# Kernel tuning notes

Hardware: AMD Instinct MI355X
Metric: run time of the kernel (lower is better)

The kernel has to match this reference:

```python
import jax, jax.numpy as jnp
import numpy as np

NH, HD, MB = 32, 64, 16        # heads, head_dim, TTT mini-batch size
BASE_LR = 1.0
ROPE_THETA = 10000.0


def _ln(x, w, b, eps):
    mu = x.mean(-1, keepdims=True)
    var = ((x - mu) ** 2).mean(-1, keepdims=True)
    return (x - mu) / jnp.sqrt(var + eps) * w + b


def _rotate_half(x):
    x1, x2 = jnp.split(x, 2, axis=-1)
    return jnp.concatenate([-x2, x1], axis=-1)


def _ln_l2_bwd(x, target, g, b, eps=1e-6):
    # grad of ||LN(x)*g+b - target||^2 / 2 wrt x (fused, as in ttt-lm)
    D = x.shape[-1]
    mu = x.mean(-1, keepdims=True)
    var = ((x - mu) ** 2).mean(-1, keepdims=True)
    std = jnp.sqrt(var + eps)
    xh = (x - mu) / std
    gxh = (g * xh + b - target) * g
    return (D * gxh - gxh.sum(-1, keepdims=True) - xh * (gxh * xh).sum(-1, keepdims=True)) / (D * std)


def _ttt_forward(x, q_w, k_w, v_w, o_w, ttt_lr_w, ttt_lr_b, token_idx_off,
                 ttt_norm_w, ttt_norm_b, W1, b1, post_w, post_b):
    B, L, C = x.shape
    NM = L // MB
    XQ = (x @ q_w).reshape(B, L, NH, HD).transpose(0, 2, 1, 3)  # [B,NH,L,HD]
    XK = (x @ k_w).reshape(B, L, NH, HD).transpose(0, 2, 1, 3)
    XV = (x @ v_w).reshape(B, L, NH, HD).transpose(0, 2, 1, 3)
    # rotary embedding at position_ids % mini_batch_size
    pos = (jnp.arange(L) % MB).astype(jnp.float32)
    inv = 1.0 / (ROPE_THETA ** (jnp.arange(0, HD, 2, dtype=jnp.float32) / HD))
    fr = pos[:, None] * inv[None, :]
    emb = jnp.concatenate([fr, fr], axis=-1)           # [L,HD]
    cos, sin = jnp.cos(emb), jnp.sin(emb)
    XQ = XQ * cos + _rotate_half(XQ) * sin
    XK = XK * cos + _rotate_half(XK) * sin
    # learning-rate gate (eta)
    Xm = x.reshape(B, NM, MB, C)
    ttt_lr = jax.nn.sigmoid(jnp.einsum('bnkc,hdc->bhnkd', Xm, ttt_lr_w)
                            + ttt_lr_b.reshape(1, NH, 1, 1, 1))       # [B,NH,NM,MB,1]
    ttt_lr_eta = BASE_LR * ttt_lr.transpose(0, 1, 2, 4, 3) / HD       # [B,NH,NM,1,MB]
    tok = jnp.maximum(1.0 / jnp.arange(1, MB + 1, dtype=jnp.float32) + token_idx_off, 0.0)
    eta = tok.reshape(1, 1, 1, MB, 1) * ttt_lr_eta                    # [B,NH,NM,MB,MB]

    def tomb(t):  # [B,NH,L,HD] -> [NM,B,NH,MB,HD]
        return t.reshape(B, NH, NM, MB, HD).transpose(2, 0, 1, 3, 4)

    xs = (tomb(XQ), tomb(XK), tomb(XV), eta.transpose(2, 0, 1, 3, 4))
    lw = ttt_norm_w.reshape(1, NH, 1, HD)
    lb = ttt_norm_b.reshape(1, NH, 1, HD)
    tril = jnp.tril(jnp.ones((MB, MB), x.dtype))
    W1s = jnp.broadcast_to(W1, (B, NH, HD, HD)).astype(x.dtype)
    b1s = jnp.broadcast_to(b1, (B, NH, 1, HD)).astype(x.dtype)

    def step(carry, xs_t):
        W1c, b1c = carry
        xq, xk, xv, et = xs_t                      # [B,NH,MB,HD], et [B,NH,MB,MB]
        Z1 = xk @ W1c + b1c
        grad = _ln_l2_bwd(Z1, xv - xk, lw, lb)     # grad of per-head TTT loss wrt Z1
        Attn1 = jnp.tril(xq @ xk.transpose(0, 1, 3, 2))
        b1_bar = b1c - (et * tril) @ grad
        Z1_bar = xq @ W1c - (et * Attn1) @ grad + b1_bar
        last_eta = et[:, :, -1, :, None]           # [B,NH,MB,1]
        W1n = W1c - jnp.einsum('bhki,bhkj->bhij', last_eta * xk, grad)
        b1n = b1c - (last_eta * grad).sum(-2, keepdims=True)
        out = xq + _ln(Z1_bar, lw, lb, 1e-6)
        return (W1n, b1n), out

    _, outs = jax.lax.scan(step, (W1s, b1s), xs)   # outs: [NM,B,NH,MB,HD]
    y = outs.transpose(1, 0, 3, 2, 4).reshape(B, L, C)
    y = _ln(y, post_w, post_b, 1e-6)
    return y @ o_w


def setup_inputs() -> dict:
    key = jax.random.key(0)
    ks = jax.random.split(key, 16)
    B, L, C, DH = 4, 2048, 2048, 1024
    s = 0.02
    return {
        'enc_input': jax.random.normal(ks[0], (B, L, C), jnp.float32),
        'ln1_w': jnp.ones((C,), jnp.float32), 'ln1_b': jnp.zeros((C,), jnp.float32),
        'q_w': jax.random.normal(ks[1], (C, C), jnp.float32) * s,
        'k_w': jax.random.normal(ks[2], (C, C), jnp.float32) * s,
        'v_w': jax.random.normal(ks[3], (C, C), jnp.float32) * s,
        'o_w': jax.random.normal(ks[4], (C, C), jnp.float32) * s,
        'ttt_lr_w': jax.random.normal(ks[5], (NH, 1, C), jnp.float32) * s,
        'ttt_lr_b': jax.random.normal(ks[6], (NH,), jnp.float32) * s,
        'token_idx_off': jax.random.normal(ks[7], (MB,), jnp.float32) * 0.01,
        'ttt_norm_w': jnp.ones((NH, HD), jnp.float32),
        'ttt_norm_b': jnp.zeros((NH, HD), jnp.float32),
        'W1': jax.random.normal(ks[8], (NH, HD, HD), jnp.float32) * s,
        'b1': jnp.zeros((NH, 1, HD), jnp.float32),
        'post_w': jnp.ones((C,), jnp.float32), 'post_b': jnp.zeros((C,), jnp.float32),
        'ffn_ln_w': jnp.ones((C,), jnp.float32), 'ffn_ln_b': jnp.zeros((C,), jnp.float32),
        'w1f': jax.random.normal(ks[9], (C, DH), jnp.float32) * s,
        'b1f': jnp.zeros((DH,), jnp.float32),
        'w2f': jax.random.normal(ks[10], (DH, C), jnp.float32) * s,
        'b2f': jnp.zeros((C,), jnp.float32),
    }


def reference(enc_input, ln1_w, ln1_b, q_w, k_w, v_w, o_w, ttt_lr_w, ttt_lr_b,
              token_idx_off, ttt_norm_w, ttt_norm_b, W1, b1, post_w, post_b,
              ffn_ln_w, ffn_ln_b, w1f, b1f, w2f, b2f):
    # pre-LN (torch default eps=1e-5) + TTT linear block + residual
    x = _ln(enc_input, ln1_w, ln1_b, 1e-5)
    y = _ttt_forward(x, q_w, k_w, v_w, o_w, ttt_lr_w, ttt_lr_b, token_idx_off,
                     ttt_norm_w, ttt_norm_b, W1, b1, post_w, post_b)
    y = y + enc_input
    # position-wise FFN (pre-LN eps=1e-6) + residual; dropout = eval no-op
    z = _ln(y, ffn_ln_w, ffn_ln_b, 1e-6)
    z = jax.nn.relu(z @ w1f + b1f) @ w2f + b2f
    return z + y
```

## Files before the change

### kernel.cpp

```cpp
#include <hip/hip_runtime.h>

typedef unsigned short u16;
typedef __attribute__((ext_vector_type(8))) short short8;
typedef __attribute__((ext_vector_type(8))) unsigned short ushort8;
typedef __attribute__((ext_vector_type(4))) unsigned short us4;
typedef __attribute__((ext_vector_type(4))) float f32x4;
typedef __attribute__((ext_vector_type(2))) float f32x2;
typedef __attribute__((ext_vector_type(2))) unsigned int uint2v;

#define DEV __device__ __forceinline__

DEV float bf2f(u16 u){ union{unsigned int i; float f;} v; v.i = ((unsigned int)u)<<16u; return v.f; }
DEV u16 f2bf(float f){ union{float f; unsigned int i;} v; v.f=f; unsigned int r = v.i + 0x7FFFu + ((v.i>>16)&1u); return (u16)(r>>16); }

DEV void gload16(const u16* g, u16* l){
  __builtin_amdgcn_global_load_lds((const __attribute__((address_space(1))) void*)g,
                                   (__attribute__((address_space(3))) void*)l, 16, 0, 0);
}

DEV float wsum(float v){
  v += __shfl_xor(v, 32, 64);
  v += __shfl_xor(v, 16, 64);
  v += __shfl_xor(v, 8, 64);
  v += __shfl_xor(v, 4, 64);
  v += __shfl_xor(v, 2, 64);
  v += __shfl_xor(v, 1, 64);
  return v;
}

#if __has_builtin(__builtin_amdgcn_permlane16_swap) && __has_builtin(__builtin_amdgcn_permlane32_swap)
DEV float qsum(float v){
  unsigned u = __float_as_uint(v);
  uint2v a = __builtin_amdgcn_permlane16_swap(u, u, false, false);
  float s = __uint_as_float(a[0]) + __uint_as_float(a[1]);
  unsigned u2 = __float_as_uint(s);
  uint2v bsw = __builtin_amdgcn_permlane32_swap(u2, u2, false, false);
  return __uint_as_float(bsw[0]) + __uint_as_float(bsw[1]);
}
#else
DEV float qsum(float v){
  v += __shfl_xor(v, 16, 64);
  v += __shfl_xor(v, 32, 64);
  return v;
}
#endif

DEV float swap32(float v){ return __shfl_xor(v, 32, 64); }

#define BARS() do{ asm volatile("s_waitcnt lgkmcnt(0)" ::: "memory"); \
  __builtin_amdgcn_s_barrier(); __builtin_amdgcn_sched_barrier(0); }while(0)

__global__ __launch_bounds__(256) void ln_row(
    const float* __restrict__ in, const float* __restrict__ w, const float* __restrict__ bb,
    float eps, u16* __restrict__ outb)
{
  const int wv = threadIdx.x>>6, lane = threadIdx.x&63;
  const int row = blockIdx.x*4 + wv;
  const float* p = in + (size_t)row*2048 + lane*4;
  f32x4 a[8];
  #pragma unroll
  for(int j=0;j<8;j++) a[j] = *(const f32x4*)(p + j*256);
  float s = 0.f;
  #pragma unroll
  for(int j=0;j<8;j++) s += a[j][0]+a[j][1]+a[j][2]+a[j][3];
  s = wsum(s);
  float mu = s*(1.f/2048.f);
  float vs = 0.f;
  #pragma unroll
  for(int j=0;j<8;j++)
    #pragma unroll
    for(int r=0;r<4;r++){ float d=a[j][r]-mu; vs += d*d; }
  vs = wsum(vs);
  float rstd = rsqrtf(vs*(1.f/2048.f) + eps);
  #pragma unroll
  for(int j=0;j<8;j++){
    f32x4 wj = *(const f32x4*)(w  + j*256 + lane*4);
    f32x4 bj = *(const f32x4*)(bb + j*256 + lane*4);
    us4 o;
    #pragma unroll
    for(int r=0;r<4;r++) o[r] = f2bf((a[j][r]-mu)*rstd*wj[r] + bj[r]);
    *(us4*)(outb + (size_t)row*2048 + j*256 + lane*4) = o;
  }
}

__global__ __launch_bounds__(256) void transpose_cast(
    const float* __restrict__ src, u16* __restrict__ dst, int K, int N)
{
  __shared__ float tile[32][33];
  const int kb = blockIdx.x*32, nb = blockIdx.y*32;
  const int tx = threadIdx.x & 31, ty = threadIdx.x >> 5;
  #pragma unroll
  for(int i=0;i<4;i++){
    int k = ty + i*8;
    tile[k][tx] = src[(size_t)(kb+k)*N + nb + tx];
  }
  __syncthreads();
  #pragma unroll
  for(int i=0;i<4;i++){
    int nn = ty + i*8;
    dst[(size_t)(nb+nn)*K + kb + tx] = f2bf(tile[tx][nn]);
  }
}

__global__ __launch_bounds__(256) void cast_lrw(const float* __restrict__ lrw, u16* __restrict__ dst)
{
  int i = blockIdx.x*256 + threadIdx.x;
  if (i < 32*2048) dst[i] = f2bf(lrw[i]);
  else dst[i] = 0;
}

__global__ void rope_init(const float* __restrict__ tio, float* __restrict__ cosb,
                          float* __restrict__ sinb, float* __restrict__ tokb)
{
  int t = blockIdx.x*256 + threadIdx.x;
  if (t < 1024){
    int p = t>>6, d = t&63;
    float inv = powf(10000.f, -(float)(2*(d&31))/64.f);
    float fr = (float)p * inv;
    cosb[t] = cosf(fr);
    sinb[t] = sinf(fr);
  }
  if (blockIdx.x==0 && threadIdx.x<16)
    tokb[threadIdx.x] = fmaxf(1.f/(float)(threadIdx.x+1) + tio[threadIdx.x], 0.f);
}

#define MM(MI,NI,AA,BB) acc[MI][NI] = __builtin_amdgcn_mfma_f32_16x16x32_bf16(AA, BB, acc[MI][NI], 0, 0, 0)

#define RD_A(D,KH,MF) (*(const short8*)(ldsb + ((D)<<16) + ((KH)<<14) + (wm<<13) + ((MF)<<10) + loff))
#define RD_B(D,KH,NF) (*(const short8*)(ldsb + ((D)<<16) + 32768 + ((KH)<<14) + (wn<<12) + ((NF)<<10) + loff))

#define PHASE(D,KH,MH,RB,STG,VM) { \
  __builtin_amdgcn_sched_barrier(0); \
  if (RB){ b0 = RD_B(D,KH,0); b1 = RD_B(D,KH,1); b2 = RD_B(D,KH,2); b3 = RD_B(D,KH,3); } \
  short8 a0 = RD_A(D,KH,4*(MH)+0); \
  short8 a1 = RD_A(D,KH,4*(MH)+1); \
  short8 a2 = RD_A(D,KH,4*(MH)+2); \
  short8 a3 = RD_A(D,KH,4*(MH)+3); \
  STG; \
  __builtin_amdgcn_sched_barrier(0); \
  __builtin_amdgcn_s_barrier(); \
  asm volatile("s_waitcnt lgkmcnt(0)" ::: "memory"); \
  __builtin_amdgcn_sched_barrier(0); \
  __builtin_amdgcn_s_setprio(1); \
  MM(4*(MH)+0,0,a0,b0); MM(4*(MH)+1,0,a1,b0); MM(4*(MH)+2,0,a2,b0); MM(4*(MH)+3,0,a3,b0); \
  MM(4*(MH)+0,1,a0,b1); MM(4*(MH)+1,1,a1,b1); MM(4*(MH)+2,1,a2,b1); MM(4*(MH)+3,1,a3,b1); \
  MM(4*(MH)+0,2,a0,b2); MM(4*(MH)+1,2,a1,b2); MM(4*(MH)+2,2,a2,b2); MM(4*(MH)+3,2,a3,b2); \
  MM(4*(MH)+0,3,a0,b3); MM(4*(MH)+1,3,a1,b3); MM(4*(MH)+2,3,a2,b3); MM(4*(MH)+3,3,a3,b3); \
  __builtin_amdgcn_s_setprio(0); \
  if (VM){ asm volatile("s_waitcnt vmcnt(8)" ::: "memory"); } \
  __builtin_amdgcn_sched_barrier(0); \
  __builtin_amdgcn_s_barrier(); \
}

template<int EPI>
__global__ __launch_bounds__(512, 2) void gemm256(
    const u16* __restrict__ A, const u16* __restrict__ Bt,
    float* __restrict__ C, u16* __restrict__ Cb,
    const float* __restrict__ bias, const float* __restrict__ resid,
    int Nld, int Nreal, int K, int ntN)
{
  extern __shared__ u16 lds[];
  const int t = threadIdx.x, lane = t&63, wv = t>>6;
  const int wm = wv>>2, wn = wv&3;
  const int fr = lane&15, kq = lane>>4;

  int bid = blockIdx.x;
  {
    int nwg = gridDim.x;
    int q = nwg>>3, r = nwg&7;
    int x = bid&7, l = bid>>3;
    bid = (x<r) ? (x*(q+1)+l) : (r*(q+1)+(x-r)*q+l);
  }
  const int bm = bid/ntN, bn = bid%ntN;

  f32x4 acc[8][4];
  #pragma unroll
  for(int i=0;i<8;i++)
    #pragma unroll
    for(int j=0;j<4;j++) acc[i][j]=(f32x4){0.f,0.f,0.f,0.f};

  const u16* gA = A  + (size_t)(bm*256)*K;
  const u16* gB = Bt + (size_t)(bn*256)*K;

  const int Ls   = (t&7) ^ ((t>>3)&7);
  const int rstg = ((t>>3)<<1) | (Ls>>2);
  const int cstg = (Ls&3)<<3;
  u16* const ldsw = lds + (wv<<9);

  const int Plane = (((fr&1)<<2) | kq) ^ (fr>>1);
  const int loff  = ((fr>>1)<<7) | (Plane<<4);
  const char* const ldsb = (const char*)lds;

  auto stA = [&](int d, int kh, int kts){
    u16* lb = ldsw + (d<<15) + (kh<<13);
    const u16* g = gA + (size_t)rstg*K + kts + (kh<<5) + cstg;
    gload16(g, lb);
    gload16(g + ((size_t)K<<7), lb + 4096);
  };
  auto stB = [&](int d, int kh, int kts){
    u16* lb = ldsw + (d<<15) + 16384 + (kh<<13);
    const u16* g = gB + (size_t)rstg*K + kts + (kh<<5) + cstg;
    gload16(g, lb);
    gload16(g + ((size_t)K<<7), lb + 4096);
  };

  stA(0,0,0); stB(0,0,0); stA(0,1,0); stB(0,1,0); stA(1,0,64); stB(1,0,64);
  asm volatile("s_waitcnt vmcnt(8)" ::: "memory");
  __builtin_amdgcn_sched_barrier(0);
  __builtin_amdgcn_s_barrier();

  for (int kt = 0; kt < K; kt += 128){
    const int ktp = (kt+128 < K) ? kt+128 : 0;
    const int ktq = (kt+192 < K) ? kt+192 : kt+192-K;
    short8 b0={0},b1={0},b2={0},b3={0};
    PHASE(0,0,0,1, stA(1,1,kt+64), 0)
    PHASE(0,0,1,0, stB(1,1,kt+64), 1)
    PHASE(0,1,0,1, stA(0,0,ktp),   0)
    PHASE(0,1,1,0, stB(0,0,ktp),   1)
    PHASE(1,0,0,1, stA(0,1,ktp),   0)
    PHASE(1,0,1,0, stB(0,1,ktp),   1)
    PHASE(1,1,0,1, stA(1,0,ktq),   0)
    PHASE(1,1,1,0, stB(1,0,ktq),   1)
  }

  const int cr = (lane>>4)<<2, cc = lane&15;
  #pragma unroll
  for(int mi=0;mi<8;mi++){
    #pragma unroll
    for(int ni=0;ni<4;ni++){
      const int row0 = bm*256 + wm*128 + mi*16 + cr;
      const int col  = bn*256 + wn*64  + ni*16 + cc;
      if (col < Nreal){
        #pragma unroll
        for(int rr=0;rr<4;rr++){
          size_t idx = (size_t)(row0+rr)*Nld + col;
          float v = acc[mi][ni][rr];
          if (EPI==1 || EPI==3) v += resid[idx];
          if (EPI==2 || EPI==3) v += bias[col];
          if (EPI==2){ v = fmaxf(v, 0.f); Cb[idx] = f2bf(v); }
          else if (EPI==4){ Cb[idx] = f2bf(v); }
          else C[idx] = v;
        }
      }
    }
  }
}

#define W1LD 72
#define XLD  72
#define GTLD 40
#define EKLD 40
#define EALD 40
#define TD2  68

__global__ __launch_bounds__(512, 1) void ttt_scan(
    const u16* __restrict__ XQKV,
    const float* __restrict__ ropec, const float* __restrict__ ropes,
    const float* __restrict__ tokp,
    const float* __restrict__ nw, const float* __restrict__ nb,
    const float* __restrict__ lrb,
    const float* __restrict__ W1i,
    const float* __restrict__ b1i,
    float* __restrict__ Y)
{
  const int blk = blockIdx.x, b = blk>>5, h = blk&31;
  const int t = threadIdx.x, lane = t&63, wv = t>>6;
  const int fr = lane&15, quad = lane>>4;
  const bool isStager = (wv==2)||(wv==3)||(wv==5)||(wv==6);
  const int sm = (wv>=5)? wv-3 : wv-2;

  __shared__ u16 W1bf[2][64*W1LD];
  __shared__ u16 xqbf[3][16*XLD];
  __shared__ u16 xkbf[3][16*XLD];
  __shared__ u16 exkT[3][64*EKLD];
  __shared__ u16 gradTbf[2][64*GTLD];
  __shared__ u16 etaA[2][16*EALD];
  __shared__ float tgT2[3][16*TD2];
  __shared__ float xqT2[3][16*TD2];
  __shared__ float b1s[64];
  __shared__ float lrs[3][16];

  const float lrbh = lrb[h];
  const float ct = tokp[15]*(1.f/64.f);
  const float sg = (lane<32)? -1.f : 1.f;

  f32x2 lwr[16];
  #pragma unroll
  for(int m=0;m<4;m++)
    #pragma unroll
    for(int r=0;r<4;r++){
      int d = m*16+quad*4+r;
      lwr[m*4+r] = (f32x2){nw[h*64+d], nb[h*64+d]};
    }
  float tki[4];
  #pragma unroll
  for(int r=0;r<4;r++) tki[r] = tokp[quad*4+r];

  float ccj[4], ssj[4];
  f32x4 wf0, wf1, wf2, wf3;
  u16 Pq[4], Pk[4], Pv[4], Pl[4];
  if (isStager){
    #pragma unroll
    for(int j=0;j<4;j++){
      ccj[j] = ropec[(sm*4+j)*64 + lane];
      ssj[j] = ropes[(sm*4+j)*64 + lane];
    }
    const float* wsrc = W1i + (size_t)h*4096;
    #pragma unroll
    for(int r=0;r<4;r++){
      int d = sm*16+quad*4+r;
      wf0[r] = wsrc[( 0+fr)*64 + d];
      wf1[r] = wsrc[(16+fr)*64 + d];
      wf2[r] = wsrc[(32+fr)*64 + d];
      wf3[r] = wsrc[(48+fr)*64 + d];
    }
    #pragma unroll
    for(int r=0;r<4;r++){
      int d = sm*16+quad*4+r;
      W1bf[0][d*W1LD +  0 + fr] = f2bf(wf0[r]);
      W1bf[0][d*W1LD + 16 + fr] = f2bf(wf1[r]);
      W1bf[0][d*W1LD + 32 + fr] = f2bf(wf2[r]);
      W1bf[0][d*W1LD + 48 + fr] = f2bf(wf3[r]);
    }
  }
  for(int i=t;i<64*24;i+=512){
    int rr=i/24, cp=16+i%24;
    gradTbf[0][rr*GTLD+cp]=0; gradTbf[1][rr*GTLD+cp]=0;
    exkT[0][rr*EKLD+cp]=0; exkT[1][rr*EKLD+cp]=0; exkT[2][rr*EKLD+cp]=0;
  }
  for(int i=t;i<16*24;i+=512){
    int rr=i/24, cp=16+i%24;
    etaA[0][rr*EALD+cp]=0; etaA[1][rr*EALD+cp]=0;
  }
  if (t<64) b1s[t]=b1i[h*64+t];

  auto loadP = [&](int n){
    const size_t rb = (size_t)b*2048 + n*16;
    #pragma unroll
    for(int j=0;j<4;j++){
      const u16* p = XQKV + (rb+sm*4+j)*6272 + h*64 + lane;
      Pq[j]=p[0]; Pk[j]=p[2048]; Pv[j]=p[4096];
      Pl[j]=XQKV[(rb+sm*4+j)*6272 + 6144 + h];
    }
  };
  auto stage4 = [&](int slot){
    #pragma unroll
    for(int j=0;j<4;j++){
      const int i = sm*4+j;
      float q=bf2f(Pq[j]), k=bf2f(Pk[j]), v=bf2f(Pv[j]);
      float qr = q*ccj[j] + sg*swap32(q)*ssj[j];
      float kr = k*ccj[j] + sg*swap32(k)*ssj[j];
      float lr = 1.f/(1.f + expf(-(bf2f(Pl[j]) + lrbh)));
      xqbf[slot][i*XLD+lane] = f2bf(qr);
      xkbf[slot][i*XLD+lane] = f2bf(kr);
      exkT[slot][lane*EKLD+i] = f2bf(-ct*lr*kr);
      tgT2[slot][i*TD2+lane] = v - kr;
      xqT2[slot][i*TD2+lane] = qr;
      if (lane==0) lrs[slot][i]=lr;
    }
  };

  if (isStager){
    loadP(0);
    stage4(0);
    loadP(1);
  }
  __syncthreads();

  const f32x4 fzero = (f32x4){0.f,0.f,0.f,0.f};

  f32x4 zqP0=fzero, zqP1=fzero, zqP2=fzero, zqP3=fzero;
  f32x4 b1qP0=fzero, b1qP1=fzero, b1qP2=fzero, b1qP3=fzero;

  auto do_out = [&](int p2, int p3, size_t rb){
    short8 be = *(const short8*)&etaA[p2][fr*EALD + quad*8];
    f32x4 c20,c21,c22,c23;
    c20 = __builtin_amdgcn_mfma_f32_16x16x32_bf16(*(const short8*)&gradTbf[p2][( 0+fr)*GTLD + quad*8], be, fzero, 0,0,0);
    c21 = __builtin_amdgcn_mfma_f32_16x16x32_bf16(*(const short8*)&gradTbf[p2][(16+fr)*GTLD + quad*8], be, fzero, 0,0,0);
    c22 = __builtin_amdgcn_mfma_f32_16x16x32_bf16(*(const short8*)&gradTbf[p2][(32+fr)*GTLD + quad*8], be, fzero, 0,0,0);
    c23 = __builtin_amdgcn_mfma_f32_16x16x32_bf16(*(const short8*)&gradTbf[p2][(48+fr)*GTLD + quad*8], be, fzero, 0,0,0);
    f32x4 xqv0 = *(const f32x4*)&xqT2[p3][fr*TD2 +  0 + quad*4];
    f32x4 xqv1 = *(const f32x4*)&xqT2[p3][fr*TD2 + 16 + quad*4];
    f32x4 xqv2 = *(const f32x4*)&xqT2[p3][fr*TD2 + 32 + quad*4];
    f32x4 xqv3 = *(const f32x4*)&xqT2[p3][fr*TD2 + 48 + quad*4];
    f32x4 zb0,zb1,zb2,zb3;
    float s1=0.f, s2=0.f;
    #pragma unroll
    for(int r=0;r<4;r++){
      zb0[r] = zqP0[r] + b1qP0[r] + c20[r];
      zb1[r] = zqP1[r] + b1qP1[r] + c21[r];
      zb2[r] = zqP2[r] + b1qP2[r] + c22[r];
      zb3[r] = zqP3[r] + b1qP3[r] + c23[r];
      s1 += zb0[r]+zb1[r]+zb2[r]+zb3[r];
      s2 += zb0[r]*zb0[r]+zb1[r]*zb1[r]+zb2[r]*zb2[r]+zb3[r]*zb3[r];
    }
    s1 = qsum(s1); s2 = qsum(s2);
    float mu = s1*(1.f/64.f);
    float var = s2*(1.f/64.f) - mu*mu;
    float rstd = rsqrtf(var + 1e-6f);
    #pragma unroll
    for(int m=0;m<4;m++){
      f32x4* zp = (m==0)?&zb0:(m==1)?&zb1:(m==2)?&zb2:&zb3;
      const f32x4* xp = (m==0)?&xqv0:(m==1)?&xqv1:(m==2)?&xqv2:&xqv3;
      f32x4 o;
      #pragma unroll
      for(int r=0;r<4;r++){
        f32x2 wb = lwr[m*4+r];
        float xh = ((*zp)[r] - mu)*rstd;
        o[r] = (*xp)[r] + xh*wb[0] + wb[1];
      }
      *(f32x4*)&Y[(rb+fr)*2048 + h*64 + m*16 + quad*4] = o;
    }
  };

  int c3 = 0;
  for(int n=0;n<128;n++){
    const int cur2 = n&1, pb2 = cur2^1;
    const int cur3 = c3;
    const int nxt3 = (c3==2)? 0 : c3+1;
    const int pb3  = (c3==0)? 2 : c3-1;
    const size_t rbase = (size_t)b*2048 + n*16;

    if (wv < 2){
      f32x4 b1v0 = *(const f32x4*)&b1s[ 0+quad*4];
      f32x4 b1v1 = *(const f32x4*)&b1s[16+quad*4];
      f32x4 b1v2 = *(const f32x4*)&b1s[32+quad*4];
      f32x4 b1v3 = *(const f32x4*)&b1s[48+quad*4];
      f32x4 tgv0 = *(const f32x4*)&tgT2[cur3][fr*TD2 +  0 + quad*4];
      f32x4 tgv1 = *(const f32x4*)&tgT2[cur3][fr*TD2 + 16 + quad*4];
      f32x4 tgv2 = *(const f32x4*)&tgT2[cur3][fr*TD2 + 32 + quad*4];
      f32x4 tgv3 = *(const f32x4*)&tgT2[cur3][fr*TD2 + 48 + quad*4];
      short8 bk0 = *(const short8*)&xkbf[cur3][fr*XLD + quad*8];
      short8 bk1 = *(const short8*)&xkbf[cur3][fr*XLD + 32 + quad*8];
      f32x4 z0,z1,z2,z3;
      z0 = __builtin_amdgcn_mfma_f32_16x16x32_bf16(*(const short8*)&W1bf[cur2][( 0+fr)*W1LD + quad*8],      bk0, fzero, 0,0,0);
      z0 = __builtin_amdgcn_mfma_f32_16x16x32_bf16(*(const short8*)&W1bf[cur2][( 0+fr)*W1LD + 32 + quad*8], bk1, z0,    0,0,0);
      z1 = __builtin_amdgcn_mfma_f32_16x16x32_bf16(*(const short8*)&W1bf[cur2][(16+fr)*W1LD + quad*8],      bk0, fzero, 0,0,0);
      z1 = __builtin_amdgcn_mfma_f32_16x16x32_bf16(*(const short8*)&W1bf[cur2][(16+fr)*W1LD + 32 + quad*8], bk1, z1,    0,0,0);
      z2 = __builtin_amdgcn_mfma_f32_16x16x32_bf16(*(const short8*)&W1bf[cur2][(32+fr)*W1LD + quad*8],      bk0, fzero, 0,0,0);
      z2 = __builtin_amdgcn_mfma_f32_16x16x32_bf16(*(const short8*)&W1bf[cur2][(32+fr)*W1LD + 32 + quad*8], bk1, z2,    0,0,0);
      z3 = __builtin_amdgcn_mfma_f32_16x16x32_bf16(*(const short8*)&W1bf[cur2][(48+fr)*W1LD + quad*8],      bk0, fzero, 0,0,0);
      z3 = __builtin_amdgcn_mfma_f32_16x16x32_bf16(*(const short8*)&W1bf[cur2][(48+fr)*W1LD + 32 + quad*8], bk1, z3,    0,0,0);
      f32x4 xh0,xh1,xh2,xh3;
      {
        float s1=0.f, s2=0.f;
        #pragma unroll
        for(int r=0;r<4;r++){
          z0[r] += b1v0[r];
          z1[r] += b1v1[r];
          z2[r] += b1v2[r];
          z3[r] += b1v3[r];
          s1 += z0[r]+z1[r]+z2[r]+z3[r];
          s2 += z0[r]*z0[r]+z1[r]*z1[r]+z2[r]*z2[r]+z3[r]*z3[r];
        }
        s1 = qsum(s1); s2 = qsum(s2);
        float mu = s1*(1.f/64.f);
        float var = s2*(1.f/64.f) - mu*mu;
        float rstd = rsqrtf(var + 1e-6f);
        float u1=0.f, u2=0.f;
        #pragma unroll
        for(int m=0;m<4;m++){
          f32x4* zp = (m==0)?&z0:(m==1)?&z1:(m==2)?&z2:&z3;
          f32x4* xp = (m==0)?&xh0:(m==1)?&xh1:(m==2)?&xh2:&xh3;
          const f32x4* tp = (m==0)?&tgv0:(m==1)?&tgv1:(m==2)?&tgv2:&tgv3;
          #pragma unroll
          for(int r=0;r<4;r++){
            f32x2 wb = lwr[m*4+r];
            float xh = ((*zp)[r] - mu)*rstd;
            float gx = (wb[0]*xh + wb[1] - (*tp)[r])*wb[0];
            (*xp)[r] = xh;
            (*zp)[r] = gx;
            u1 += gx; u2 += gx*xh;
          }
        }
        u1 = qsum(u1); u2 = qsum(u2);
        const float c64 = rstd*(1.f/64.f);
        #pragma unroll
        for(int m=0;m<4;m++){
          f32x4* zp = (m==0)?&z0:(m==1)?&z1:(m==2)?&z2:&z3;
          f32x4* xp = (m==0)?&xh0:(m==1)?&xh1:(m==2)?&xh2:&xh3;
          #pragma unroll
          for(int r=0;r<4;r++)
            (*zp)[r] = (64.f*(*zp)[r] - u1 - (*xp)[r]*u2)*c64;
        }
      }
      f32x4 zA = (wv==0)? z0 : z2;
      f32x4 zB = (wv==0)? z1 : z3;
      const int rb0 = wv*32;
      #pragma unroll
      for(int r=0;r<4;r++){
        gradTbf[cur2][(rb0+quad*4+r)*GTLD + fr]    = f2bf(zA[r]);
        gradTbf[cur2][(rb0+16+quad*4+r)*GTLD + fr] = f2bf(zB[r]);
      }
    }
    else if (wv == 4){
      short8 bq0 = *(const short8*)&xqbf[cur3][fr*XLD + quad*8];
      short8 bq1 = *(const short8*)&xqbf[cur3][fr*XLD + 32 + quad*8];
      f32x4 zqN0,zqN1,zqN2,zqN3;
      zqN0 = __builtin_amdgcn_mfma_f32_16x16x32_bf16(*(const short8*)&W1bf[cur2][( 0+fr)*W1LD + quad*8],      bq0, fzero, 0,0,0);
      zqN0 = __builtin_amdgcn_mfma_f32_16x16x32_bf16(*(const short8*)&W1bf[cur2][( 0+fr)*W1LD + 32 + quad*8], bq1, zqN0,  0,0,0);
      zqN1 = __builtin_amdgcn_mfma_f32_16x16x32_bf16(*(const short8*)&W1bf[cur2][(16+fr)*W1LD + quad*8],      bq0, fzero, 0,0,0);
      zqN1 = __builtin_amdgcn_mfma_f32_16x16x32_bf16(*(const short8*)&W1bf[cur2][(16+fr)*W1LD + 32 + quad*8], bq1, zqN1,  0,0,0);
      zqN2 = __builtin_amdgcn_mfma_f32_16x16x32_bf16(*(const short8*)&W1bf[cur2][(32+fr)*W1LD + quad*8],      bq0, fzero, 0,0,0);
      zqN2 = __builtin_amdgcn_mfma_f32_16x16x32_bf16(*(const short8*)&W1bf[cur2][(32+fr)*W1LD + 32 + quad*8], bq1, zqN2,  0,0,0);
      zqN3 = __builtin_amdgcn_mfma_f32_16x16x32_bf16(*(const short8*)&W1bf[cur2][(48+fr)*W1LD + quad*8],      bq0, fzero, 0,0,0);
      zqN3 = __builtin_amdgcn_mfma_f32_16x16x32_bf16(*(const short8*)&W1bf[cur2][(48+fr)*W1LD + 32 + quad*8], bq1, zqN3,  0,0,0);
      if (n > 0) do_out(pb2, pb3, rbase - 16);
      zqP0=zqN0; zqP1=zqN1; zqP2=zqN2; zqP3=zqN3;
      b1qP0 = *(const f32x4*)&b1s[ 0+quad*4];
      b1qP1 = *(const f32x4*)&b1s[16+quad*4];
      b1qP2 = *(const f32x4*)&b1s[32+quad*4];
      b1qP3 = *(const f32x4*)&b1s[48+quad*4];
    }
    else if (wv == 7){
      short8 aq0 = *(const short8*)&xqbf[cur3][fr*XLD + quad*8];
      short8 aq1 = *(const short8*)&xqbf[cur3][fr*XLD + 32 + quad*8];
      short8 bk0 = *(const short8*)&xkbf[cur3][fr*XLD + quad*8];
      short8 bk1 = *(const short8*)&xkbf[cur3][fr*XLD + 32 + quad*8];
      f32x4 at;
      at = __builtin_amdgcn_mfma_f32_16x16x32_bf16(aq0, bk0, fzero, 0,0,0);
      at = __builtin_amdgcn_mfma_f32_16x16x32_bf16(aq1, bk1, at,    0,0,0);
      float lrj = lrs[cur3][fr]*(1.f/64.f);
      #pragma unroll
      for(int r=0;r<4;r++){
        int i = quad*4 + r;
        float val = (fr <= i) ? -tki[r]*lrj*(1.f + at[r]) : 0.f;
        etaA[cur2][i*EALD + fr] = f2bf(val);
      }
    }
    else {
      if (n < 127) stage4(nxt3);
      if (n < 126) loadP(n+2);
    }
    BARS();

    if (isStager){
      short8 ga = *(const short8*)&gradTbf[cur2][(sm*16+fr)*GTLD + quad*8];
      short8 e0 = *(const short8*)&exkT[cur3][( 0+fr)*EKLD + quad*8];
      short8 e1 = *(const short8*)&exkT[cur3][(16+fr)*EKLD + quad*8];
      short8 e2 = *(const short8*)&exkT[cur3][(32+fr)*EKLD + quad*8];
      short8 e3 = *(const short8*)&exkT[cur3][(48+fr)*EKLD + quad*8];
      wf0 = __builtin_amdgcn_mfma_f32_16x16x32_bf16(ga, e0, wf0, 0,0,0);
      wf1 = __builtin_amdgcn_mfma_f32_16x16x32_bf16(ga, e1, wf1, 0,0,0);
      wf2 = __builtin_amdgcn_mfma_f32_16x16x32_bf16(ga, e2, wf2, 0,0,0);
      wf3 = __builtin_amdgcn_mfma_f32_16x16x32_bf16(ga, e3, wf3, 0,0,0);
      #pragma unroll
      for(int r=0;r<4;r++){
        int d = sm*16+quad*4+r;
        W1bf[pb2][d*W1LD +  0 + fr] = f2bf(wf0[r]);
        W1bf[pb2][d*W1LD + 16 + fr] = f2bf(wf1[r]);
        W1bf[pb2][d*W1LD + 32 + fr] = f2bf(wf2[r]);
        W1bf[pb2][d*W1LD + 48 + fr] = f2bf(wf3[r]);
      }
    }
    else if (wv == 7){
      const int d = lane;
      short8 g0 = *(const short8*)&gradTbf[cur2][d*GTLD + 0];
      short8 g1 = *(const short8*)&gradTbf[cur2][d*GTLD + 8];
      float s = 0.f;
      #pragma unroll
      for(int j=0;j<8;j++) s += lrs[cur3][j]   * bf2f((u16)g0[j]);
      #pragma unroll
      for(int j=0;j<8;j++) s += lrs[cur3][8+j] * bf2f((u16)g1[j]);
      b1s[d] -= ct * s;
    }
    BARS();
    c3 = nxt3;
  }

  if (wv == 4) do_out(1, 1, (size_t)b*2048 + 127*16);
}

extern "C" void kernel_launch(void* const* d_in, const int* in_sizes, int n_in,
                              void* d_out, int out_size, void* d_ws, size_t ws_size,
                              hipStream_t stream)
{
  const float* enc   = (const float*)d_in[0];
  const float* ln1w  = (const float*)d_in[1];
  const float* ln1b  = (const float*)d_in[2];
  const float* qw    = (const float*)d_in[3];
  const float* kw    = (const float*)d_in[4];
  const float* vw    = (const float*)d_in[5];
  const float* ow    = (const float*)d_in[6];
  const float* lrw   = (const float*)d_in[7];
  const float* lrb   = (const float*)d_in[8];
  const float* tio   = (const float*)d_in[9];
  const float* tnw   = (const float*)d_in[10];
  const float* tnb   = (const float*)d_in[11];
  const float* W1i   = (const float*)d_in[12];
  const float* b1i   = (const float*)d_in[13];
  const float* postw = (const float*)d_in[14];
  const float* postb = (const float*)d_in[15];
  const float* flnw  = (const float*)d_in[16];
  const float* flnb  = (const float*)d_in[17];
  const float* w1f   = (const float*)d_in[18];
  const float* b1f   = (const float*)d_in[19];
  const float* w2f   = (const float*)d_in[20];
  const float* b2f   = (const float*)d_in[21];
  float* out = (float*)d_out;

  char* ws = (char*)d_ws;
  size_t off = 0;
  auto alloc = [&](size_t bytes)->void*{ void* p = ws + off; off += (bytes + 255) & ~(size_t)255; return p; };
  u16*   regA  = (u16*)  alloc(8192ull*2048*2);
  u16*   wqkvT = (u16*)  alloc(6400ull*2048*2);
  u16*   XQKV  = (u16*)  alloc(8192ull*6272*2);
  float* yb    = (float*)alloc(8192ull*2048*4);
  float* ropec = (float*)alloc(1024*4);
  float* ropes = (float*)alloc(1024*4);
  float* tokb  = (float*)alloc(64*4);

  u16* oT   = wqkvT;
  u16* w1fT = wqkvT + 2048ull*2048;
  u16* w2fT = w1fT + 1024ull*2048;
  u16* hbf  = XQKV;
  float* y2 = yb;

  static bool s_attr = false;
  if (!s_attr){
    s_attr = true;
    (void)hipFuncSetAttribute(reinterpret_cast<const void*>(gemm256<4>), hipFuncAttributeMaxDynamicSharedMemorySize, 131072);
    (void)hipFuncSetAttribute(reinterpret_cast<const void*>(gemm256<1>), hipFuncAttributeMaxDynamicSharedMemorySize, 131072);
    (void)hipFuncSetAttribute(reinterpret_cast<const void*>(gemm256<2>), hipFuncAttributeMaxDynamicSharedMemorySize, 131072);
    (void)hipFuncSetAttribute(reinterpret_cast<const void*>(gemm256<3>), hipFuncAttributeMaxDynamicSharedMemorySize, 131072);
  }

  rope_init<<<4, 256, 0, stream>>>(tio, ropec, ropes, tokb);

  dim3 tg1(64, 64);
  transpose_cast<<<tg1, 256, 0, stream>>>(qw, wqkvT,               2048, 2048);
  transpose_cast<<<tg1, 256, 0, stream>>>(kw, wqkvT + 2048ull*2048, 2048, 2048);
  transpose_cast<<<tg1, 256, 0, stream>>>(vw, wqkvT + 4096ull*2048, 2048, 2048);
  cast_lrw<<<2048, 256, 0, stream>>>(lrw, wqkvT + 6144ull*2048);

  ln_row<<<2048, 256, 0, stream>>>(enc, ln1w, ln1b, 1e-5f, regA);

  gemm256<4><<<32*25, 512, 131072, stream>>>(regA, wqkvT, nullptr, XQKV,
                                             nullptr, nullptr, 6272, 6272, 2048, 25);

  transpose_cast<<<tg1, 256, 0, stream>>>(ow, oT, 2048, 2048);
  dim3 tg2(64, 32);
  transpose_cast<<<tg2, 256, 0, stream>>>(w1f, w1fT, 2048, 1024);
  dim3 tg3(32, 64);
  transpose_cast<<<tg3, 256, 0, stream>>>(w2f, w2fT, 1024, 2048);

  ttt_scan<<<128, 512, 0, stream>>>(XQKV, ropec, ropes, tokb, tnw, tnb, lrb, W1i, b1i, yb);

  ln_row<<<2048, 256, 0, stream>>>(yb, postw, postb, 1e-6f, regA);
  gemm256<1><<<32*8, 512, 131072, stream>>>(regA, oT, y2, nullptr,
                                            nullptr, enc, 2048, 2048, 2048, 8);

  ln_row<<<2048, 256, 0, stream>>>(y2, flnw, flnb, 1e-6f, regA);
  gemm256<2><<<32*4, 512, 131072, stream>>>(regA, w1fT, nullptr, hbf,
                                            b1f, nullptr, 1024, 1024, 2048, 4);
  gemm256<3><<<32*8, 512, 131072, stream>>>(hbf, w2fT, out, nullptr,
                                            b2f, y2, 2048, 2048, 1024, 8);
}
```

Before: 768.6 us.

## Merge TTT scan W1 update into gradient waves and drop second barrier

The per-minibatch loop in the TTT scan now has waves 0-3 each compute one gradient slice, write it, and then apply their own W1 MFMA update in the same phase. The b1 update is done with a lane shuffle reduction into a double-buffered b1 array, which removes the second block barrier per iteration. Staging moves to waves 5-7 with 6/6/4 rows each, and wave 7 also builds the eta matrix. The six weight transpose-cast launches are batched into two grid-z launches. The risk is a longer critical path on waves 0-3 and heavier register use in the staging waves.

```diff
diff --git a/kernel.cpp b/kernel.cpp
--- a/kernel.cpp
+++ b/kernel.cpp
@@ -45,6 +45,14 @@
 }
 #endif
 
+DEV float jsum(float v){
+  v += __shfl_xor(v, 1, 64);
+  v += __shfl_xor(v, 2, 64);
+  v += __shfl_xor(v, 4, 64);
+  v += __shfl_xor(v, 8, 64);
+  return v;
+}
+
 DEV float swap32(float v){ return __shfl_xor(v, 32, 64); }
 
 #define BARS() do{ asm volatile("s_waitcnt lgkmcnt(0)" ::: "memory"); \
@@ -83,11 +91,19 @@
   }
 }
 
-__global__ __launch_bounds__(256) void transpose_cast(
-    const float* __restrict__ src, u16* __restrict__ dst, int K, int N)
+__global__ __launch_bounds__(256) void transpose_cast3(
+    const float* __restrict__ s0, u16* __restrict__ d0v, int K0, int N0,
+    const float* __restrict__ s1, u16* __restrict__ d1v, int K1, int N1,
+    const float* __restrict__ s2, u16* __restrict__ d2v, int K2, int N2)
 {
+  const int z = blockIdx.z;
+  const float* src = (z==0)? s0 : (z==1)? s1 : s2;
+  u16* dst = (z==0)? d0v : (z==1)? d1v : d2v;
+  const int K = (z==0)? K0 : (z==1)? K1 : K2;
+  const int N = (z==0)? N0 : (z==1)? N1 : N2;
+  const int kb = blockIdx.x*32, nb = blockIdx.y*32;
+  if (kb >= K || nb >= N) return;
   __shared__ float tile[32][33];
-  const int kb = blockIdx.x*32, nb = blockIdx.y*32;
   const int tx = threadIdx.x & 31, ty = threadIdx.x >> 5;
   #pragma unroll
   for(int i=0;i<4;i++){
@@ -266,8 +282,9 @@
   const int blk = blockIdx.x, b = blk>>5, h = blk&31;
   const int t = threadIdx.x, lane = t&63, wv = t>>6;
   const int fr = lane&15, quad = lane>>4;
-  const bool isStager = (wv==2)||(wv==3)||(wv==5)||(wv==6);
-  const int sm = (wv>=5)? wv-3 : wv-2;
+  const bool isStager = (wv>=5);
+  const int nrows = (wv==7)? 4 : 6;
+  const int row0 = (wv==5)? 0 : (wv==6)? 6 : 12;
 
   __shared__ u16 W1bf[2][64*W1LD];
   __shared__ u16 xqbf[3][16*XLD];
@@ -277,7 +294,7 @@
   __shared__ u16 etaA[2][16*EALD];
   __shared__ float tgT2[3][16*TD2];
   __shared__ float xqT2[3][16*TD2];
-  __shared__ float b1s[64];
+  __shared__ float b1s[2][64];
   __shared__ float lrs[3][16];
 
   const float lrbh = lrb[h];
@@ -296,19 +313,12 @@
   #pragma unroll
   for(int r=0;r<4;r++) tki[r] = tokp[quad*4+r];
 
-  float ccj[4], ssj[4];
   f32x4 wf0, wf1, wf2, wf3;
-  u16 Pq[4], Pk[4], Pv[4], Pl[4];
-  if (isStager){
-    #pragma unroll
-    for(int j=0;j<4;j++){
-      ccj[j] = ropec[(sm*4+j)*64 + lane];
-      ssj[j] = ropes[(sm*4+j)*64 + lane];
-    }
+  if (wv < 4){
     const float* wsrc = W1i + (size_t)h*4096;
     #pragma unroll
     for(int r=0;r<4;r++){
-      int d = sm*16+quad*4+r;
+      int d = wv*16+quad*4+r;
       wf0[r] = wsrc[( 0+fr)*64 + d];
       wf1[r] = wsrc[(16+fr)*64 + d];
       wf2[r] = wsrc[(32+fr)*64 + d];
@@ -316,13 +326,22 @@
     }
     #pragma unroll
     for(int r=0;r<4;r++){
-      int d = sm*16+quad*4+r;
+      int d = wv*16+quad*4+r;
       W1bf[0][d*W1LD +  0 + fr] = f2bf(wf0[r]);
       W1bf[0][d*W1LD + 16 + fr] = f2bf(wf1[r]);
       W1bf[0][d*W1LD + 32 + fr] = f2bf(wf2[r]);
       W1bf[0][d*W1LD + 48 + fr] = f2bf(wf3[r]);
     }
   }
+  float ccj[6], ssj[6];
+  u16 Pq[6], Pk[6], Pv[6], Pl[6];
+  if (isStager){
+    #pragma unroll
+    for(int j=0;j<6;j++) if (j < nrows){
+      ccj[j] = ropec[(row0+j)*64 + lane];
+      ssj[j] = ropes[(row0+j)*64 + lane];
+    }
+  }
   for(int i=t;i<64*24;i+=512){
     int rr=i/24, cp=16+i%24;
     gradTbf[0][rr*GTLD+cp]=0; gradTbf[1][rr*GTLD+cp]=0;
@@ -332,21 +351,21 @@
     int rr=i/24, cp=16+i%24;
     etaA[0][rr*EALD+cp]=0; etaA[1][rr*EALD+cp]=0;
   }
-  if (t<64) b1s[t]=b1i[h*64+t];
+  if (t<64) b1s[0][t]=b1i[h*64+t];
 
   auto loadP = [&](int n){
     const size_t rb = (size_t)b*2048 + n*16;
     #pragma unroll
-    for(int j=0;j<4;j++){
-      const u16* p = XQKV + (rb+sm*4+j)*6272 + h*64 + lane;
+    for(int j=0;j<6;j++) if (j < nrows){
+      const u16* p = XQKV + (rb+row0+j)*6272 + h*64 + lane;
       Pq[j]=p[0]; Pk[j]=p[2048]; Pv[j]=p[4096];
-      Pl[j]=XQKV[(rb+sm*4+j)*6272 + 6144 + h];
+      Pl[j]=XQKV[(rb+row0+j)*6272 + 6144 + h];
     }
   };
-  auto stage4 = [&](int slot){
-    #pragma unroll
-    for(int j=0;j<4;j++){
-      const int i = sm*4+j;
+  auto stageN = [&](int slot){
+    #pragma unroll
+    for(int j=0;j<6;j++) if (j < nrows){
+      const int i = row0+j;
       float q=bf2f(Pq[j]), k=bf2f(Pk[j]), v=bf2f(Pv[j]);
       float qr = q*ccj[j] + sg*swap32(q)*ssj[j];
       float kr = k*ccj[j] + sg*swap32(k)*ssj[j];
@@ -362,7 +381,7 @@
 
   if (isStager){
     loadP(0);
-    stage4(0);
+    stageN(0);
     loadP(1);
   }
   __syncthreads();
@@ -421,11 +440,11 @@
     const int pb3  = (c3==0)? 2 : c3-1;
     const size_t rbase = (size_t)b*2048 + n*16;
 
-    if (wv < 2){
-      f32x4 b1v0 = *(const f32x4*)&b1s[ 0+quad*4];
-      f32x4 b1v1 = *(const f32x4*)&b1s[16+quad*4];
-      f32x4 b1v2 = *(const f32x4*)&b1s[32+quad*4];
-      f32x4 b1v3 = *(const f32x4*)&b1s[48+quad*4];
+    if (wv < 4){
+      f32x4 b1v0 = *(const f32x4*)&b1s[cur2][ 0+quad*4];
+      f32x4 b1v1 = *(const f32x4*)&b1s[cur2][16+quad*4];
+      f32x4 b1v2 = *(const f32x4*)&b1s[cur2][32+quad*4];
+      f32x4 b1v3 = *(const f32x4*)&b1s[cur2][48+quad*4];
       f32x4 tgv0 = *(const f32x4*)&tgT2[cur3][fr*TD2 +  0 + quad*4];
       f32x4 tgv1 = *(const f32x4*)&tgT2[cur3][fr*TD2 + 16 + quad*4];
       f32x4 tgv2 = *(const f32x4*)&tgT2[cur3][fr*TD2 + 32 + quad*4];
@@ -484,13 +503,39 @@
             (*zp)[r] = (64.f*(*zp)[r] - u1 - (*xp)[r]*u2)*c64;
         }
       }
-      f32x4 zA = (wv==0)? z0 : z2;
-      f32x4 zB = (wv==0)? z1 : z3;
-      const int rb0 = wv*32;
+      f32x4 zsel = (wv==0)?z0:(wv==1)?z1:(wv==2)?z2:z3;
+      #pragma unroll
+      for(int r=0;r<4;r++)
+        gradTbf[cur2][(wv*16+quad*4+r)*GTLD + fr] = f2bf(zsel[r]);
+      {
+        float ej = ct * lrs[cur3][fr];
+        f32x4 del;
+        #pragma unroll
+        for(int r=0;r<4;r++) del[r] = jsum(ej * zsel[r]);
+        f32x4 b1own = (wv==0)?b1v0:(wv==1)?b1v1:(wv==2)?b1v2:b1v3;
+        if (fr == 0){
+          #pragma unroll
+          for(int r=0;r<4;r++) b1s[pb2][wv*16+quad*4+r] = b1own[r] - del[r];
+        }
+      }
+      asm volatile("s_waitcnt lgkmcnt(0)" ::: "memory");
+      __builtin_amdgcn_sched_barrier(0);
+      short8 ga = *(const short8*)&gradTbf[cur2][(wv*16+fr)*GTLD + quad*8];
+      short8 e0 = *(const short8*)&exkT[cur3][( 0+fr)*EKLD + quad*8];
+      short8 e1 = *(const short8*)&exkT[cur3][(16+fr)*EKLD + quad*8];
+      short8 e2 = *(const short8*)&exkT[cur3][(32+fr)*EKLD + quad*8];
+      short8 e3 = *(const short8*)&exkT[cur3][(48+fr)*EKLD + quad*8];
+      wf0 = __builtin_amdgcn_mfma_f32_16x16x32_bf16(ga, e0, wf0, 0,0,0);
+      wf1 = __builtin_amdgcn_mfma_f32_16x16x32_bf16(ga, e1, wf1, 0,0,0);
+      wf2 = __builtin_amdgcn_mfma_f32_16x16x32_bf16(ga, e2, wf2, 0,0,0);
+      wf3 = __builtin_amdgcn_mfma_f32_16x16x32_bf16(ga, e3, wf3, 0,0,0);
       #pragma unroll
       for(int r=0;r<4;r++){
-        gradTbf[cur2][(rb0+quad*4+r)*GTLD + fr]    = f2bf(zA[r]);
-        gradTbf[cur2][(rb0+16+quad*4+r)*GTLD + fr] = f2bf(zB[r]);
+        int d = wv*16+quad*4+r;
+        W1bf[pb2][d*W1LD +  0 + fr] = f2bf(wf0[r]);
+        W1bf[pb2][d*W1LD + 16 + fr] = f2bf(wf1[r]);
+        W1bf[pb2][d*W1LD + 32 + fr] = f2bf(wf2[r]);
+        W1bf[pb2][d*W1LD + 48 + fr] = f2bf(wf3[r]);
       }
     }
     else if (wv == 4){
@@ -507,62 +552,30 @@
       zqN3 = __builtin_amdgcn_mfma_f32_16x16x32_bf16(*(const short8*)&W1bf[cur2][(48+fr)*W1LD + 32 + quad*8], bq1, zqN3,  0,0,0);
       if (n > 0) do_out(pb2, pb3, rbase - 16);
       zqP0=zqN0; zqP1=zqN1; zqP2=zqN2; zqP3=zqN3;
-      b1qP0 = *(const f32x4*)&b1s[ 0+quad*4];
-      b1qP1 = *(const f32x4*)&b1s[16+quad*4];
-      b1qP2 = *(const f32x4*)&b1s[32+quad*4];
-      b1qP3 = *(const f32x4*)&b1s[48+quad*4];
-    }
-    else if (wv == 7){
-      short8 aq0 = *(const short8*)&xqbf[cur3][fr*XLD + quad*8];
-      short8 aq1 = *(const short8*)&xqbf[cur3][fr*XLD + 32 + quad*8];
-      short8 bk0 = *(const short8*)&xkbf[cur3][fr*XLD + quad*8];
-      short8 bk1 = *(const short8*)&xkbf[cur3][fr*XLD + 32 + quad*8];
-      f32x4 at;
-      at = __builtin_amdgcn_mfma_f32_16x16x32_bf16(aq0, bk0, fzero, 0,0,0);
-      at = __builtin_amdgcn_mfma_f32_16x16x32_bf16(aq1, bk1, at,    0,0,0);
-      float lrj = lrs[cur3][fr]*(1.f/64.f);
-      #pragma unroll
-      for(int r=0;r<4;r++){
-        int i = quad*4 + r;
-        float val = (fr <= i) ? -tki[r]*lrj*(1.f + at[r]) : 0.f;
-        etaA[cur2][i*EALD + fr] = f2bf(val);
+      b1qP0 = *(const f32x4*)&b1s[cur2][ 0+quad*4];
+      b1qP1 = *(const f32x4*)&b1s[cur2][16+quad*4];
+      b1qP2 = *(const f32x4*)&b1s[cur2][32+quad*4];
+      b1qP3 = *(const f32x4*)&b1s[cur2][48+quad*4];
+    }
+    else {
+      if (wv == 7){
+        short8 aq0 = *(const short8*)&xqbf[cur3][fr*XLD + quad*8];
+        short8 aq1 = *(const short8*)&xqbf[cur3][fr*XLD + 32 + quad*8];
+        short8 bk0 = *(const short8*)&xkbf[cur3][fr*XLD + quad*8];
+        short8 bk1 = *(const short8*)&xkbf[cur3][fr*XLD + 32 + quad*8];
+        f32x4 at;
+        at = __builtin_amdgcn_mfma_f32_16x16x32_bf16(aq0, bk0, fzero, 0,0,0);
+        at = __builtin_amdgcn_mfma_f32_16x16x32_bf16(aq1, bk1, at,    0,0,0);
+        float lrj = lrs[cur3][fr]*(1.f/64.f);
+        #pragma unroll
+        for(int r=0;r<4;r++){
+          int i = quad*4 + r;
+          float val = (fr <= i) ? -tki[r]*lrj*(1.f + at[r]) : 0.f;
+          etaA[cur2][i*EALD + fr] = f2bf(val);
+        }
       }
-    }
-    else {
-      if (n < 127) stage4(nxt3);
+      if (n < 127) stageN(nxt3);
       if (n < 126) loadP(n+2);
-    }
-    BARS();
-
-    if (isStager){
-      short8 ga = *(const short8*)&gradTbf[cur2][(sm*16+fr)*GTLD + quad*8];
-      short8 e0 = *(const short8*)&exkT[cur3][( 0+fr)*EKLD + quad*8];
-      short8 e1 = *(const short8*)&exkT[cur3][(16+fr)*EKLD + quad*8];
-      short8 e2 = *(const short8*)&exkT[cur3][(32+fr)*EKLD + quad*8];
-      short8 e3 = *(const short8*)&exkT[cur3][(48+fr)*EKLD + quad*8];
-      wf0 = __builtin_amdgcn_mfma_f32_16x16x32_bf16(ga, e0, wf0, 0,0,0);
-      wf1 = __builtin_amdgcn_mfma_f32_16x16x32_bf16(ga, e1, wf1, 0,0,0);
-      wf2 = __builtin_amdgcn_mfma_f32_16x16x32_bf16(ga, e2, wf2, 0,0,0);
-      wf3 = __builtin_amdgcn_mfma_f32_16x16x32_bf16(ga, e3, wf3, 0,0,0);
-      #pragma unroll
-      for(int r=0;r<4;r++){
-        int d = sm*16+quad*4+r;
-        W1bf[pb2][d*W1LD +  0 + fr] = f2bf(wf0[r]);
-        W1bf[pb2][d*W1LD + 16 + fr] = f2bf(wf1[r]);
-        W1bf[pb2][d*W1LD + 32 + fr] = f2bf(wf2[r]);
-        W1bf[pb2][d*W1LD + 48 + fr] = f2bf(wf3[r]);
-      }
-    }
-    else if (wv == 7){
-      const int d = lane;
-      short8 g0 = *(const short8*)&gradTbf[cur2][d*GTLD + 0];
-      short8 g1 = *(const short8*)&gradTbf[cur2][d*GTLD + 8];
-      float s = 0.f;
-      #pragma unroll
-      for(int j=0;j<8;j++) s += lrs[cur3][j]   * bf2f((u16)g0[j]);
-      #pragma unroll
-      for(int j=0;j<8;j++) s += lrs[cur3][8+j] * bf2f((u16)g1[j]);
-      b1s[d] -= ct * s;
     }
     BARS();
     c3 = nxt3;
@@ -627,10 +640,10 @@
 
   rope_init<<<4, 256, 0, stream>>>(tio, ropec, ropes, tokb);
 
-  dim3 tg1(64, 64);
-  transpose_cast<<<tg1, 256, 0, stream>>>(qw, wqkvT,               2048, 2048);
-  transpose_cast<<<tg1, 256, 0, stream>>>(kw, wqkvT + 2048ull*2048, 2048, 2048);
-  transpose_cast<<<tg1, 256, 0, stream>>>(vw, wqkvT + 4096ull*2048, 2048, 2048);
+  transpose_cast3<<<dim3(64,64,3), 256, 0, stream>>>(
+      qw, wqkvT,                2048, 2048,
+      kw, wqkvT + 2048ull*2048, 2048, 2048,
+      vw, wqkvT + 4096ull*2048, 2048, 2048);
   cast_lrw<<<2048, 256, 0, stream>>>(lrw, wqkvT + 6144ull*2048);
 
   ln_row<<<2048, 256, 0, stream>>>(enc, ln1w, ln1b, 1e-5f, regA);
@@ -638,11 +651,10 @@
   gemm256<4><<<32*25, 512, 131072, stream>>>(regA, wqkvT, nullptr, XQKV,
                                              nullptr, nullptr, 6272, 6272, 2048, 25);
 
-  transpose_cast<<<tg1, 256, 0, stream>>>(ow, oT, 2048, 2048);
-  dim3 tg2(64, 32);
-  transpose_cast<<<tg2, 256, 0, stream>>>(w1f, w1fT, 2048, 1024);
-  dim3 tg3(32, 64);
-  transpose_cast<<<tg3, 256, 0, stream>>>(w2f, w2fT, 1024, 2048);
+  transpose_cast3<<<dim3(64,64,3), 256, 0, stream>>>(
+      ow,  oT,   2048, 2048,
+      w1f, w1fT, 2048, 1024,
+      w2f, w2fT, 1024, 2048);
 
   ttt_scan<<<128, 512, 0, stream>>>(XQKV, ropec, ropes, tokb, tnw, tnb, lrb, W1i, b1i, yb);
 
```

After: 763.9 us. About the same (-0.6%).
